# Kernel optimization log

Hardware: AMD Instinct MI355X
Metric: run time of the kernel (lower is better)

## Reference

```python
import jax, jax.numpy as jnp
import numpy as np

B, T, D, A = 64, 2048, 512, 128

def setup_inputs() -> dict:
    key = jax.random.key(0)
    k_x, k_w1, k_b1, k_w2, k_b2 = jax.random.split(key, 5)
    s1 = 1.0 / np.sqrt(D)
    s2 = 1.0 / np.sqrt(A)
    return {
        "x": jax.random.normal(k_x, (B, T, D), dtype=jnp.float32),
        "W1": jax.random.uniform(k_w1, (D, A), minval=-s1, maxval=s1, dtype=jnp.float32),
        "b1": jax.random.uniform(k_b1, (A,), minval=-s1, maxval=s1, dtype=jnp.float32),
        "W2": jax.random.uniform(k_w2, (A, 1), minval=-s2, maxval=s2, dtype=jnp.float32),
        "b2": jax.random.uniform(k_b2, (1,), minval=-s2, maxval=s2, dtype=jnp.float32),
    }

def reference(x, W1, b1, W2, b2):
    # attention scores: [B, T, 1]
    h = jnp.tanh(jnp.einsum('btd,da->bta', x, W1) + b1)
    scores = jnp.einsum('bta,ao->bto', h, W2) + b2
    w = jax.nn.softmax(scores, axis=1)              # [B, T, 1]
    mu = jnp.sum(x * w, axis=1)                     # [B, D]
    var = jnp.sum((x - mu[:, None, :]) ** 2 * w, axis=1)
    std = jnp.sqrt(var + 1e-6)
    return jnp.concatenate([mu, std], axis=-1)      # [B, 2D]
```

## Files before the change

kernel.cpp:

```cpp
#include <hip/hip_runtime.h>
#include <hip/hip_bf16.h>
#include <math.h>

#define B_ 64
#define T_ 2048
#define D_ 512
#define A_ 128

#define CHUNK  32
#define NCHUNK 8
#define SEG    (CHUNK*NCHUNK)
#define NBLK   (B_*(T_/SEG))

typedef __bf16 bf16x8 __attribute__((ext_vector_type(8)));
typedef float  f32x4  __attribute__((ext_vector_type(4)));

__global__ __launch_bounds__(256) void prep_kernel(
    const float* __restrict__ W1, __hip_bfloat16* __restrict__ W1T)
{
    int idx = blockIdx.x * 256 + threadIdx.x;
    int k = idx >> 7;
    int n = idx & 127;
    W1T[n * D_ + k] = __float2bfloat16(W1[idx]);
}

__device__ inline bf16x8 cvt8(float4 a, float4 b) {
    bf16x8 r;
    r[0] = (__bf16)a.x; r[1] = (__bf16)a.y; r[2] = (__bf16)a.z; r[3] = (__bf16)a.w;
    r[4] = (__bf16)b.x; r[5] = (__bf16)b.y; r[6] = (__bf16)b.z; r[7] = (__bf16)b.w;
    return r;
}

__device__ inline float fast_tanh(float v) {
    v = fminf(fmaxf(v, -15.f), 15.f);
    float e = __expf(2.f * v);
    return (e - 1.f) / (e + 1.f);
}

typedef __attribute__((address_space(1))) const void gas_t;
typedef __attribute__((address_space(3))) void las_t;
#define GLOAD_LDS16(g, l) \
    __builtin_amdgcn_global_load_lds((gas_t*)(g), (las_t*)(l), 16, 0, 0)

__global__ __launch_bounds__(256, 1) void fused_kernel(
    const float* __restrict__ x, const __hip_bfloat16* __restrict__ W1T_,
    const float* __restrict__ b1, const float* __restrict__ W2,
    const float* __restrict__ b2,
    float* __restrict__ pS, float* __restrict__ pmu, float* __restrict__ pm2)
{
    __shared__ __align__(16) float xs[2][CHUNK * D_];
    __shared__ float parr[4][2][16];
    __shared__ float uarr[CHUNK];

    const __bf16* W1T = (const __bf16*)W1T_;
    const int tid  = threadIdx.x;
    const int wv   = tid >> 6;
    const int lane = tid & 63;
    const int col  = lane & 15;
    const int kgrp = lane >> 4;

    const int bk  = blockIdx.x;
    const int b   = bk >> 3;
    const int seg = bk & 7;
    const float* xb = x + ((long)b * T_ + (long)seg * SEG) * D_;

    bf16x8 af[2][16];
#pragma unroll
    for (int mtl = 0; mtl < 2; mtl++) {
        const __bf16* wp = W1T + (long)((2*wv + mtl)*16 + col) * D_ + kgrp*8;
#pragma unroll
        for (int ks = 0; ks < 16; ks++)
            af[mtl][ks] = *(const bf16x8*)(wp + ks*32);
    }
    float b1v[2][4], w2v[2][4];
#pragma unroll
    for (int mtl = 0; mtl < 2; mtl++)
#pragma unroll
        for (int r = 0; r < 4; r++) {
            int n = (2*wv + mtl)*16 + kgrp*4 + r;
            b1v[mtl][r] = b1[n];
            w2v[mtl][r] = W2[n];
        }
    const float bias2 = b2[0];

    float mu0 = 0.f, mu1 = 0.f, m20 = 0.f, m21 = 0.f, su = 0.f;

    auto STAGE = [&](int bufi, int c) {
        const float* src = xb + (long)c * (CHUNK * D_);
        float* dstbase = &xs[bufi][0];
#pragma unroll
        for (int j = 0; j < 16; j++) {
            int G = j*256 + tid;
            int t = G >> 7;
            int g = G & 127;
            const float* gp = src + t*D_ + ((g ^ (t & 7)) << 2);
            float* lp = dstbase + ((j*256 + wv*64) << 2);
            GLOAD_LDS16(gp, lp);
        }
    };

    STAGE(0, 0);
    int cur = 0;

    for (int c = 0; c < NCHUNK; c++) {
        if (c + 1 < NCHUNK) {
            STAGE(cur ^ 1, c + 1);
            asm volatile("s_waitcnt vmcnt(16)" ::: "memory");
        } else {
            asm volatile("s_waitcnt vmcnt(0)" ::: "memory");
        }
        __builtin_amdgcn_s_barrier();
        asm volatile("" ::: "memory");

        const float* bufp = &xs[cur][0];

        f32x4 acc[2][2];
#pragma unroll
        for (int mtl = 0; mtl < 2; mtl++)
#pragma unroll
            for (int tt = 0; tt < 2; tt++)
                acc[mtl][tt] = (f32x4){0.f, 0.f, 0.f, 0.f};

#pragma unroll
        for (int ks = 0; ks < 16; ks++) {
            bf16x8 bfr[2];
#pragma unroll
            for (int tt = 0; tt < 2; tt++) {
                int t  = tt*16 + col;
                int m  = t & 7;
                int gb = ks*8 + kgrp*2;
                float4 aa = *(const float4*)(bufp + (t << 9) + (((gb    ) ^ m) << 2));
                float4 bb = *(const float4*)(bufp + (t << 9) + (((gb + 1) ^ m) << 2));
                bfr[tt] = cvt8(aa, bb);
            }
#pragma unroll
            for (int mtl = 0; mtl < 2; mtl++) {
                acc[mtl][0] = __builtin_amdgcn_mfma_f32_16x16x32_bf16(af[mtl][ks], bfr[0], acc[mtl][0], 0, 0, 0);
                acc[mtl][1] = __builtin_amdgcn_mfma_f32_16x16x32_bf16(af[mtl][ks], bfr[1], acc[mtl][1], 0, 0, 0);
            }
        }

        float p0 = 0.f, p1 = 0.f;
#pragma unroll
        for (int mtl = 0; mtl < 2; mtl++)
#pragma unroll
            for (int r = 0; r < 4; r++) {
                p0 += fast_tanh(acc[mtl][0][r] + b1v[mtl][r]) * w2v[mtl][r];
                p1 += fast_tanh(acc[mtl][1][r] + b1v[mtl][r]) * w2v[mtl][r];
            }
        p0 += __shfl_xor(p0, 16, 64);
        p0 += __shfl_xor(p0, 32, 64);
        p1 += __shfl_xor(p1, 16, 64);
        p1 += __shfl_xor(p1, 32, 64);
        if (lane < 16) {
            parr[wv][0][lane] = p0;
            parr[wv][1][lane] = p1;
        }
        asm volatile("s_waitcnt lgkmcnt(0)" ::: "memory");
        __builtin_amdgcn_s_barrier();
        asm volatile("" ::: "memory");

        if (tid < CHUNK) {
            int tt = tid >> 4, cc = tid & 15;
            float s = parr[0][tt][cc] + parr[1][tt][cc]
                    + parr[2][tt][cc] + parr[3][tt][cc] + bias2;
            uarr[tid] = __expf(s);
        }
        asm volatile("s_waitcnt lgkmcnt(0)" ::: "memory");
        __builtin_amdgcn_s_barrier();
        asm volatile("" ::: "memory");

        const int gacc = tid >> 1;
        const int fo   = (tid & 1) << 1;
#pragma unroll
        for (int t = 0; t < CHUNK; t++) {
            float u = uarr[t];
            const float* pp = bufp + (t << 9) + ((gacc ^ (t & 7)) << 2) + fo;
            float2 xv = *(const float2*)pp;
            mu0 = fmaf(u, xv.x, mu0);
            mu1 = fmaf(u, xv.y, mu1);
            m20 = fmaf(u * xv.x, xv.x, m20);
            m21 = fmaf(u * xv.y, xv.y, m21);
            su += u;
        }
        asm volatile("" ::: "memory");
        __builtin_amdgcn_s_barrier();
        asm volatile("" ::: "memory");

        cur ^= 1;
    }

    const int d0 = tid * 2;
    pmu[(long)bk * D_ + d0]     = mu0;
    pmu[(long)bk * D_ + d0 + 1] = mu1;
    pm2[(long)bk * D_ + d0]     = m20;
    pm2[(long)bk * D_ + d0 + 1] = m21;
    if (tid == 0) pS[bk] = su;
}

__global__ __launch_bounds__(256) void merge_kernel(
    const float* __restrict__ pS, const float* __restrict__ pmu,
    const float* __restrict__ pm2, float* __restrict__ out)
{
    const int b = blockIdx.x, tid = threadIdx.x;
    float S = 0.f;
#pragma unroll
    for (int c = 0; c < 8; c++) S += pS[b*8 + c];
    const float inv = 1.f / S;

    const int d0 = tid * 2;
    float mu0 = 0.f, mu1 = 0.f, m20 = 0.f, m21 = 0.f;
#pragma unroll
    for (int c = 0; c < 8; c++) {
        const float* pb = pmu + (long)(b*8 + c) * D_ + d0;
        const float* qb = pm2 + (long)(b*8 + c) * D_ + d0;
        mu0 += pb[0]; mu1 += pb[1];
        m20 += qb[0]; m21 += qb[1];
    }
    mu0 *= inv; mu1 *= inv; m20 *= inv; m21 *= inv;

    float* ob = out + (long)b * (2 * D_);
    ob[d0]     = mu0;
    ob[d0 + 1] = mu1;
    ob[D_ + d0]     = sqrtf(fmaxf(m20 - mu0 * mu0, 0.f) + 1e-6f);
    ob[D_ + d0 + 1] = sqrtf(fmaxf(m21 - mu1 * mu1, 0.f) + 1e-6f);
}

extern "C" void kernel_launch(void* const* d_in, const int* in_sizes, int n_in,
                              void* d_out, int out_size, void* d_ws, size_t ws_size,
                              hipStream_t stream) {
    const float* x  = (const float*)d_in[0];
    const float* W1 = (const float*)d_in[1];
    const float* b1 = (const float*)d_in[2];
    const float* W2 = (const float*)d_in[3];
    const float* b2 = (const float*)d_in[4];
    float* out = (float*)d_out;

    float* ws = (float*)d_ws;
    float* pS  = ws;
    float* pmu = ws + 512;
    float* pm2 = pmu + 512L * D_;
    __hip_bfloat16* W1T = (__hip_bfloat16*)(pm2 + 512L * D_);

    prep_kernel<<<256, 256, 0, stream>>>(W1, W1T);
    fused_kernel<<<NBLK, 256, 0, stream>>>(x, W1T, b1, W2, b2, pS, pmu, pm2);
    merge_kernel<<<B_, 256, 0, stream>>>(pS, pmu, pm2, out);
}
```

Measured before the change: 387.8 us.

## Halve chunk size, allow two blocks per CU, compute softmax weights redundantly per thread

Cuts the staged chunk from 32 to 16 timesteps, which halves LDS use per block (about 64KB instead of 128KB) and lets two blocks share a CU under launch_bounds(256,2). It also removes one barrier per chunk: every thread now reads the partial scores and computes the exp weights itself instead of 32 threads writing them to shared memory. The cost is twice as many chunk iterations, with their barriers, and each MFMA pass doing half the work. There is also redundant exp work per thread and more register pressure, since the bound must now fit two blocks per CU.

```diff
diff --git a/kernel.cpp b/kernel.cpp
--- a/kernel.cpp
+++ b/kernel.cpp
@@ -7,8 +7,8 @@
 #define D_ 512
 #define A_ 128
 
-#define CHUNK  32
-#define NCHUNK 8
+#define CHUNK  16
+#define NCHUNK 16
 #define SEG    (CHUNK*NCHUNK)
 #define NBLK   (B_*(T_/SEG))
 
@@ -42,15 +42,14 @@
 #define GLOAD_LDS16(g, l) \
     __builtin_amdgcn_global_load_lds((gas_t*)(g), (las_t*)(l), 16, 0, 0)
 
-__global__ __launch_bounds__(256, 1) void fused_kernel(
+__global__ __launch_bounds__(256, 2) void fused_kernel(
     const float* __restrict__ x, const __hip_bfloat16* __restrict__ W1T_,
     const float* __restrict__ b1, const float* __restrict__ W2,
     const float* __restrict__ b2,
     float* __restrict__ pS, float* __restrict__ pmu, float* __restrict__ pm2)
 {
     __shared__ __align__(16) float xs[2][CHUNK * D_];
-    __shared__ float parr[4][2][16];
-    __shared__ float uarr[CHUNK];
+    __shared__ __align__(16) float parr[4][16];
 
     const __bf16* W1T = (const __bf16*)W1T_;
     const int tid  = threadIdx.x;
@@ -89,7 +88,7 @@
         const float* src = xb + (long)c * (CHUNK * D_);
         float* dstbase = &xs[bufi][0];
 #pragma unroll
-        for (int j = 0; j < 16; j++) {
+        for (int j = 0; j < 8; j++) {
             int G = j*256 + tid;
             int t = G >> 7;
             int g = G & 127;
@@ -105,7 +104,7 @@
     for (int c = 0; c < NCHUNK; c++) {
         if (c + 1 < NCHUNK) {
             STAGE(cur ^ 1, c + 1);
-            asm volatile("s_waitcnt vmcnt(16)" ::: "memory");
+            asm volatile("s_waitcnt vmcnt(8)" ::: "memory");
         } else {
             asm volatile("s_waitcnt vmcnt(0)" ::: "memory");
         }
@@ -114,74 +113,59 @@
 
         const float* bufp = &xs[cur][0];
 
-        f32x4 acc[2][2];
+        f32x4 acc[2];
+        acc[0] = (f32x4){0.f, 0.f, 0.f, 0.f};
+        acc[1] = (f32x4){0.f, 0.f, 0.f, 0.f};
+
+#pragma unroll
+        for (int ks = 0; ks < 16; ks++) {
+            const int m  = col & 7;
+            const int gb = ks*8 + kgrp*2;
+            float4 aa = *(const float4*)(bufp + (col << 9) + (((gb    ) ^ m) << 2));
+            float4 bb = *(const float4*)(bufp + (col << 9) + (((gb + 1) ^ m) << 2));
+            bf16x8 bfr = cvt8(aa, bb);
+            acc[0] = __builtin_amdgcn_mfma_f32_16x16x32_bf16(af[0][ks], bfr, acc[0], 0, 0, 0);
+            acc[1] = __builtin_amdgcn_mfma_f32_16x16x32_bf16(af[1][ks], bfr, acc[1], 0, 0, 0);
+        }
+
+        float p0 = 0.f;
 #pragma unroll
         for (int mtl = 0; mtl < 2; mtl++)
 #pragma unroll
-            for (int tt = 0; tt < 2; tt++)
-                acc[mtl][tt] = (f32x4){0.f, 0.f, 0.f, 0.f};
-
-#pragma unroll
-        for (int ks = 0; ks < 16; ks++) {
-            bf16x8 bfr[2];
-#pragma unroll
-            for (int tt = 0; tt < 2; tt++) {
-                int t  = tt*16 + col;
-                int m  = t & 7;
-                int gb = ks*8 + kgrp*2;
-                float4 aa = *(const float4*)(bufp + (t << 9) + (((gb    ) ^ m) << 2));
-                float4 bb = *(const float4*)(bufp + (t << 9) + (((gb + 1) ^ m) << 2));
-                bfr[tt] = cvt8(aa, bb);
-            }
-#pragma unroll
-            for (int mtl = 0; mtl < 2; mtl++) {
-                acc[mtl][0] = __builtin_amdgcn_mfma_f32_16x16x32_bf16(af[mtl][ks], bfr[0], acc[mtl][0], 0, 0, 0);
-                acc[mtl][1] = __builtin_amdgcn_mfma_f32_16x16x32_bf16(af[mtl][ks], bfr[1], acc[mtl][1], 0, 0, 0);
-            }
-        }
-
-        float p0 = 0.f, p1 = 0.f;
-#pragma unroll
-        for (int mtl = 0; mtl < 2; mtl++)
-#pragma unroll
-            for (int r = 0; r < 4; r++) {
-                p0 += fast_tanh(acc[mtl][0][r] + b1v[mtl][r]) * w2v[mtl][r];
-                p1 += fast_tanh(acc[mtl][1][r] + b1v[mtl][r]) * w2v[mtl][r];
-            }
+            for (int r = 0; r < 4; r++)
+                p0 += fast_tanh(acc[mtl][r] + b1v[mtl][r]) * w2v[mtl][r];
         p0 += __shfl_xor(p0, 16, 64);
         p0 += __shfl_xor(p0, 32, 64);
-        p1 += __shfl_xor(p1, 16, 64);
-        p1 += __shfl_xor(p1, 32, 64);
-        if (lane < 16) {
-            parr[wv][0][lane] = p0;
-            parr[wv][1][lane] = p1;
-        }
+        if (lane < 16) parr[wv][lane] = p0;
         asm volatile("s_waitcnt lgkmcnt(0)" ::: "memory");
         __builtin_amdgcn_s_barrier();
         asm volatile("" ::: "memory");
 
-        if (tid < CHUNK) {
-            int tt = tid >> 4, cc = tid & 15;
-            float s = parr[0][tt][cc] + parr[1][tt][cc]
-                    + parr[2][tt][cc] + parr[3][tt][cc] + bias2;
-            uarr[tid] = __expf(s);
-        }
-        asm volatile("s_waitcnt lgkmcnt(0)" ::: "memory");
-        __builtin_amdgcn_s_barrier();
-        asm volatile("" ::: "memory");
+        float u[16];
+#pragma unroll
+        for (int q = 0; q < 4; q++) {
+            float4 v0 = *(const float4*)&parr[0][q*4];
+            float4 v1 = *(const float4*)&parr[1][q*4];
+            float4 v2 = *(const float4*)&parr[2][q*4];
+            float4 v3 = *(const float4*)&parr[3][q*4];
+            u[q*4+0] = __expf(v0.x + v1.x + v2.x + v3.x + bias2);
+            u[q*4+1] = __expf(v0.y + v1.y + v2.y + v3.y + bias2);
+            u[q*4+2] = __expf(v0.z + v1.z + v2.z + v3.z + bias2);
+            u[q*4+3] = __expf(v0.w + v1.w + v2.w + v3.w + bias2);
+        }
+#pragma unroll
+        for (int t = 0; t < 16; t++) su += u[t];
 
         const int gacc = tid >> 1;
         const int fo   = (tid & 1) << 1;
 #pragma unroll
-        for (int t = 0; t < CHUNK; t++) {
-            float u = uarr[t];
+        for (int t = 0; t < 16; t++) {
             const float* pp = bufp + (t << 9) + ((gacc ^ (t & 7)) << 2) + fo;
             float2 xv = *(const float2*)pp;
-            mu0 = fmaf(u, xv.x, mu0);
-            mu1 = fmaf(u, xv.y, mu1);
-            m20 = fmaf(u * xv.x, xv.x, m20);
-            m21 = fmaf(u * xv.y, xv.y, m21);
-            su += u;
+            mu0 = fmaf(u[t], xv.x, mu0);
+            mu1 = fmaf(u[t], xv.y, mu1);
+            m20 = fmaf(u[t] * xv.x, xv.x, m20);
+            m21 = fmaf(u[t] * xv.y, xv.y, m21);
         }
         asm volatile("" ::: "memory");
         __builtin_amdgcn_s_barrier();
```

New measurement: 392.6 us. Within noise of the previous version (+1.2%).
